# Optimization experiments

Hardware: AMD Instinct MI355X
Metric: run time of the kernel (lower is better)

## Reference

```python
import jax, jax.numpy as jnp
import numpy as np
from jax import lax

K = 3
ALPHA = 2000.0
TAU = 0.001
MAX_ITER = 100
EPS = 1e-7


def setup_inputs() -> dict:
    key = jax.random.key(0)
    x = jax.random.normal(key, (8, 2048, 32), dtype=jnp.float32)
    return {"x": x}


def _vmd(x):
    B, L, D = x.shape
    # shifted frequency grid, identical across B and D
    f = jnp.fft.fftshift(jnp.fft.fftfreq(L)).astype(x.dtype)          # [L]
    f_bld = f[None, :, None]                                           # [1,L,1]
    # nonnegative-frequency mask; torch code boolean-masks f_shifted >= 0,
    # which is uniform over B and D, so it is a weighted sum over L here
    pos = (f >= 0).astype(x.dtype)[None, None, :, None]                # [1,1,L,1]
    x_hat = jnp.fft.fftshift(jnp.fft.fft(x, axis=1), axes=1)          # [B,L,D] complex

    def step(carry, _):
        u, omega, lam = carry  # u:[B,K,L,D], omega:[B,K,D], lam:[B,L,D]
        # Gauss-Seidel mode updates (each mode sees already-updated others)
        for k_idx in range(K):
            sum_other = jnp.sum(u, axis=1) - u[:, k_idx]               # [B,L,D]
            sum_other_hat = jnp.fft.fftshift(jnp.fft.fft(sum_other, axis=1), axes=1)
            num = x_hat - sum_other_hat + lam * 0.5                    # lam added in freq domain, as in source
            den = 1.0 + 2.0 * ALPHA * (f_bld - omega[:, k_idx][:, None, :]) ** 2
            u_k = jnp.real(jnp.fft.ifft(jnp.fft.ifftshift(num / den, axes=1), axis=1))
            u = u.at[:, k_idx].set(u_k)
        # center-frequency update over nonnegative shifted frequencies
        u_hat = jnp.fft.fftshift(jnp.fft.fft(u, axis=2), axes=2)       # [B,K,L,D]
        p = (u_hat.real ** 2 + u_hat.imag ** 2) * pos                  # |u_hat|^2 masked
        omega = jnp.sum(f[None, None, :, None] * p, axis=2) / (jnp.sum(p, axis=2) + EPS)  # [B,K,D]
        # dual ascent on lambda
        lam = lam + TAU * (x - jnp.sum(u, axis=1))
        return (u, omega, lam), None

    u0 = jnp.zeros((B, K, L, D), x.dtype)
    om0 = jnp.zeros((B, K, D), x.dtype)
    lam0 = jnp.zeros((B, L, D), x.dtype)
    (u, omega, _), _ = lax.scan(jax.checkpoint(step), (u0, om0, lam0), None, length=MAX_ITER)

    # sort modes per batch element by mean center frequency
    order = jnp.argsort(jnp.mean(omega, axis=2), axis=1)               # [B,K]
    u_sorted = jnp.take_along_axis(u, order[:, :, None, None], axis=1)
    return u_sorted[:, 0], u_sorted[:, 1], u_sorted[:, 2]


def reference(x):
    return _vmd(x)
```

## Files before the change

### kernel.cpp

```cpp
#include <hip/hip_runtime.h>

#define PD(i) ((i) + ((i) >> 5))
#define BLD 524288

__device__ __forceinline__ float2 cadd(float2 a, float2 b){ return make_float2(a.x+b.x, a.y+b.y); }
__device__ __forceinline__ float2 csub(float2 a, float2 b){ return make_float2(a.x-b.x, a.y-b.y); }
__device__ __forceinline__ float2 cmul(float2 a, float2 b){ return make_float2(a.x*b.x - a.y*b.y, a.x*b.y + a.y*b.x); }
__device__ __forceinline__ float2 cmuli(float2 a, float s){ return make_float2(-s*a.y, s*a.x); }

template<int CTRL, int RM>
__device__ __forceinline__ float dpp_add(float x){
  int r = __builtin_amdgcn_update_dpp(0, __float_as_int(x), CTRL, RM, 0xf, true);
  return x + __int_as_float(r);
}
__device__ __forceinline__ float wave_sum64(float x){
  x = dpp_add<0x111,0xf>(x);
  x = dpp_add<0x112,0xf>(x);
  x = dpp_add<0x114,0xf>(x);
  x = dpp_add<0x118,0xf>(x);
  x = dpp_add<0x142,0xa>(x);
  x = dpp_add<0x143,0xc>(x);
  return x;
}

__device__ __forceinline__ float2 exbp(int addr, float2 v){
  return make_float2(
    __int_as_float(__builtin_amdgcn_ds_bpermute(addr, __float_as_int(v.x))),
    __int_as_float(__builtin_amdgcn_ds_bpermute(addr, __float_as_int(v.y))));
}
template<int PAT>
__device__ __forceinline__ float2 exswz(float2 v){
  return make_float2(
    __int_as_float(__builtin_amdgcn_ds_swizzle(__float_as_int(v.x), PAT)),
    __int_as_float(__builtin_amdgcn_ds_swizzle(__float_as_int(v.y), PAT)));
}
template<int CTRL>
__device__ __forceinline__ float2 exdpp(float2 v){
  return make_float2(
    __int_as_float(__builtin_amdgcn_update_dpp(0, __float_as_int(v.x), CTRL, 0xF, 0xF, true)),
    __int_as_float(__builtin_amdgcn_update_dpp(0, __float_as_int(v.y), CTRL, 0xF, 0xF, true)));
}

template<int SGN>
__device__ __forceinline__ void dft8(float2 a[8]) {
  const float sgn = (float)SGN;
  const float C8 = 0.70710678118654752440f;
  float2 e0=a[0], e1=a[2], e2=a[4], e3=a[6];
  float2 o0=a[1], o1=a[3], o2=a[5], o3=a[7];
  float2 t0=cadd(e0,e2), t1=csub(e0,e2), t2=cadd(e1,e3), t3=csub(e1,e3);
  float2 E0=cadd(t0,t2), E2=csub(t0,t2);
  float2 t3i=cmuli(t3,sgn);
  float2 E1=cadd(t1,t3i), E3=csub(t1,t3i);
  float2 s0=cadd(o0,o2), s1=csub(o0,o2), s2=cadd(o1,o3), s3=csub(o1,o3);
  float2 O0=cadd(s0,s2), O2=csub(s0,s2);
  float2 s3i=cmuli(s3,sgn);
  float2 O1=cadd(s1,s3i), O3=csub(s1,s3i);
  float2 w1o = make_float2(C8*(O1.x - sgn*O1.y), C8*(O1.y + sgn*O1.x));
  float2 w2o = cmuli(O2, sgn);
  float2 w3o = make_float2(-C8*(O3.x + sgn*O3.y), C8*(sgn*O3.x - O3.y));
  a[0]=cadd(E0,O0); a[4]=csub(E0,O0);
  a[1]=cadd(E1,w1o); a[5]=csub(E1,w1o);
  a[2]=cadd(E2,w2o); a[6]=csub(E2,w2o);
  a[3]=cadd(E3,w3o); a[7]=csub(E3,w3o);
}

template<int SGN>
__device__ void fft2048(float2* bufA, float2* bufB, const float2* twd, int tid)
{
  const float sgn = (float)SGN;
  {
    float2 a[8];
    #pragma unroll
    for (int j=0;j<8;j++) a[j] = bufA[PD(tid + 256*j)];
    dft8<SGN>(a);
    float2 tw = twd[tid];
    float2 w1 = make_float2(tw.x, sgn*tw.y), wj = w1;
    #pragma unroll
    for (int j=1;j<8;j++){ a[j] = cmul(a[j], wj); wj = cmul(wj, w1); }
    #pragma unroll
    for (int j=0;j<8;j++) bufB[PD(8*tid + j)] = a[j];
  }
  __syncthreads();
  {
    float2 a[8];
    #pragma unroll
    for (int j=0;j<8;j++) a[j] = bufB[PD(tid + 256*j)];
    dft8<SGN>(a);
    int p = tid >> 3, q = tid & 7;
    float2 tw = twd[p << 3];
    float2 w1 = make_float2(tw.x, sgn*tw.y), wj = w1;
    #pragma unroll
    for (int j=1;j<8;j++){ a[j] = cmul(a[j], wj); wj = cmul(wj, w1); }
    int base = q + (p << 6);
    #pragma unroll
    for (int j=0;j<8;j++) bufA[PD(base + (j<<3))] = a[j];
  }
  __syncthreads();
  {
    float2 a[8];
    #pragma unroll
    for (int j=0;j<8;j++) a[j] = bufA[PD(tid + 256*j)];
    dft8<SGN>(a);
    int p = tid >> 6, q = tid & 63;
    float2 tw = twd[p << 6];
    float2 w1 = make_float2(tw.x, sgn*tw.y), wj = w1;
    #pragma unroll
    for (int j=1;j<8;j++){ a[j] = cmul(a[j], wj); wj = cmul(wj, w1); }
    int base = q + (p << 9);
    #pragma unroll
    for (int j=0;j<8;j++) bufB[PD(base + (j<<6))] = a[j];
  }
  __syncthreads();
  {
    #pragma unroll
    for (int h=0; h<2; h++){
      int q = tid + (h<<8);
      float2 b0 = bufB[PD(q)], b1 = bufB[PD(q+512)], b2 = bufB[PD(q+1024)], b3 = bufB[PD(q+1536)];
      float2 t0=cadd(b0,b2), t1=csub(b0,b2), t2=cadd(b1,b3), t3=csub(b1,b3);
      float2 t3i=cmuli(t3,sgn);
      bufA[PD(q)]      = cadd(t0,t2);
      bufA[PD(q+512)]  = cadd(t1,t3i);
      bufA[PD(q+1024)] = csub(t0,t2);
      bufA[PD(q+1536)] = csub(t1,t3i);
    }
  }
  __syncthreads();
}

__device__ __forceinline__ void dft4p(float2 a[4]){
  float2 t0=cadd(a[0],a[2]), t1=csub(a[0],a[2]), t2=cadd(a[1],a[3]), t3=csub(a[1],a[3]);
  float2 t3i = make_float2(-t3.y, t3.x);
  a[0]=cadd(t0,t2); a[2]=csub(t0,t2);
  a[1]=cadd(t1,t3i); a[3]=csub(t1,t3i);
}

template<bool TRANSP>
__global__ __launch_bounds__(256, 1) void vmd_main(const float* __restrict__ xg,
                                                   float* __restrict__ uout,
                                                   float* __restrict__ omout)
{
  __shared__ float2 sbufA[2112];
  __shared__ float2 sbufB[2112];
  __shared__ float2 stwd[1024];
  __shared__ float  sred[24];

  float2* sS  = sbufB;
  float2* sTY = sbufA;

  const int t = threadIdx.x;
  const int lane = t & 63;
  const int w = t >> 6;
  const int blk = blockIdx.x;
  const int b = blk >> 5;
  const int d = blk & 31;
  const float inv2048 = 1.0f/2048.0f;

  for (int j = t; j < 1024; j += 256) {
    double th = 3.14159265358979323846 * (double)j / 1024.0;
    stwd[j] = make_float2((float)cos(th), (float)sin(th));
  }

  int idxs[8];
  float fl[4];
  #pragma unroll
  for (int c = 0; c < 4; c++) {
    int iL = 4*t + c;
    idxs[c]   = iL;
    idxs[c+4] = (iL == 0) ? 1024 : (2048 - iL);
    fl[c] = (float)(iL - 1024) * inv2048;
  }

  float xv[8];
  #pragma unroll
  for (int e = 0; e < 8; e++) xv[e] = xg[(b*2048 + idxs[e])*32 + d];

  #pragma unroll
  for (int e = 0; e < 8; e++) {
    float v = (idxs[e] & 1) ? -xv[e] : xv[e];
    sbufA[PD(idxs[e])] = make_float2(v, 0.0f);
  }
  __syncthreads();
  fft2048<-1>(sbufA, sbufB, stwd, t);
  float2 X[4];
  if (t == 0) X[0] = make_float2(sbufA[PD(0)].x, sbufA[PD(1024)].x);
  else        X[0] = sbufA[PD(4*t)];
  X[1] = sbufA[PD(4*t+1)];
  X[2] = sbufA[PD(4*t+2)];
  X[3] = sbufA[PD(4*t+3)];

  int r6 = ((lane&1)<<5)|((lane&2)<<3)|((lane&4)<<1)|((lane&8)>>1)|((lane&16)>>3)|((lane&32)>>5);
  const int prb = w*528 + lane;
  float2 wq[4];
  #pragma unroll
  for (int j=0;j<4;j++) wq[j] = stwd[4*lane + 256*j + w];
  float2 w2561 = stwd[8*lane];
  float2 w2562 = stwd[16*lane & 2047] ;
  float2 w2563 = cmul(w2561, w2562);
  const float sg32 = (lane&32)?-1.f:1.f, sg16 = (lane&16)?-1.f:1.f, sg8 = (lane&8)?-1.f:1.f;
  const float sg4  = (lane&4) ?-1.f:1.f, sg2  = (lane&2) ?-1.f:1.f, sg1 = (lane&1)?-1.f:1.f;
  const float2 one = make_float2(1.f, 0.f);
  float2 tw32 = (lane&32)? stwd[32*(lane&31)]  : one;
  float2 tw16 = (lane&16)? stwd[64*(lane&15)]  : one;
  float2 tw8  = (lane&8) ? stwd[128*(lane&7)]  : one;
  float2 tw4  = (lane&4) ? stwd[256*(lane&3)]  : one;
  float2 tw2  = (lane&2) ? stwd[512*(lane&1)]  : one;
  const int bp32 = ((lane^32) << 2);
  const int tyb = w*264 + r6;
  float2 tytw[4];
  #pragma unroll
  for (int r=0;r<4;r++){
    int xx2 = 2*w*(r + 4*r6);
    tytw[r] = (xx2 < 1024) ? stwd[xx2]
            : make_float2(-stwd[xx2-1024].x, -stwd[xx2-1024].y);
  }
  int slA, slB, slC, slD, slE;
  float2 phA, phB, phC, phD, phE;
  float s2A, s2B, s2C, s2D, s2E;
  {
    int ks[5];
    ks[0] = 2*t; ks[1] = 2*t+1;
    ks[2] = (t==0) ? 512 : (1024 - 2*t);
    ks[3] = 1023 - 2*t; ks[4] = 1022 - 2*t;
    int   sl[5]; float2 ph[5]; float s2[5];
    #pragma unroll
    for (int i=0;i<5;i++){
      int k1 = ks[i] >> 8, k2 = ks[i] & 255;
      sl[i] = 66*(k2 & 3) + (k2 >> 2);
      float2 P = (k1==0)? make_float2(1,0) : (k1==1)? make_float2(0,1)
               : (k1==2)? make_float2(-1,0) : make_float2(0,-1);
      ph[i] = P; s2[i] = (k1 & 1) ? -1.f : 1.f;
    }
    slA=sl[0]; slB=sl[1]; slC=sl[2]; slD=sl[3]; slE=sl[4];
    phA=ph[0]; phB=ph[1]; phC=ph[2]; phD=ph[3]; phE=ph[4];
    s2A=s2[0]; s2B=s2[1]; s2C=s2[2]; s2D=s2[3]; s2E=s2[4];
  }

  auto stageSpec = [&](float2 v0, float2 v1, float2 v2, float2 v3){
    if (t == 0) { sS[0] = make_float2(v0.x, 0.f); sS[256] = make_float2(v0.y, 0.f); }
    else        { sS[t] = v0;                     sS[512 - t] = make_float2(v0.x, -v0.y); }
    sS[528  + t] = v1;  sS[2095 - t] = make_float2(v1.x, -v1.y);
    sS[1056 + t] = v2;  sS[1567 - t] = make_float2(v2.x, -v2.y);
    sS[1584 + t] = v3;  sS[1039 - t] = make_float2(v3.x, -v3.y);
  };

  auto runFFT = [&](){
    float2 C[4];
    #pragma unroll
    for (int j=0;j<4;j++){
      float2 lo = sS[prb + 64*j];
      float2 hi = sS[prb + 64*j + 256];
      float2 Av = cadd(lo, hi), Bv = csub(lo, hi);
      float2 WB = cmul(wq[j], Bv);
      C[j] = make_float2(Av.x - WB.y, Av.y + WB.x);
    }
    dft4p(C);
    C[1] = cmul(C[1], w2561); C[2] = cmul(C[2], w2562); C[3] = cmul(C[3], w2563);
    #pragma unroll
    for (int r=0;r<4;r++){
      float2 e = exbp(bp32, C[r]);
      C[r] = cmul(make_float2(fmaf(sg32, C[r].x, e.x), fmaf(sg32, C[r].y, e.y)), tw32);
    }
    #pragma unroll
    for (int r=0;r<4;r++){
      float2 e = exswz<0x401F>(C[r]);
      C[r] = cmul(make_float2(fmaf(sg16, C[r].x, e.x), fmaf(sg16, C[r].y, e.y)), tw16);
    }
    #pragma unroll
    for (int r=0;r<4;r++){
      float2 e = exswz<0x201F>(C[r]);
      C[r] = cmul(make_float2(fmaf(sg8, C[r].x, e.x), fmaf(sg8, C[r].y, e.y)), tw8);
    }
    #pragma unroll
    for (int r=0;r<4;r++){
      float2 e = exswz<0x101F>(C[r]);
      C[r] = cmul(make_float2(fmaf(sg4, C[r].x, e.x), fmaf(sg4, C[r].y, e.y)), tw4);
    }
    #pragma unroll
    for (int r=0;r<4;r++){
      float2 e = exdpp<0x4E>(C[r]);
      C[r] = cmul(make_float2(fmaf(sg2, C[r].x, e.x), fmaf(sg2, C[r].y, e.y)), tw2);
    }
    #pragma unroll
    for (int r=0;r<4;r++){
      float2 e = exdpp<0xB1>(C[r]);
      C[r] = make_float2(fmaf(sg1, C[r].x, e.x), fmaf(sg1, C[r].y, e.y));
    }
    #pragma unroll
    for (int r=0;r<4;r++) sTY[tyb + 66*r] = cmul(C[r], tytw[r]);
  };

  auto zread = [&](int sl, float2 phi, float s2) -> float2 {
    float2 a0 = sTY[sl], a1 = sTY[sl+264], a2 = sTY[sl+528], a3 = sTY[sl+792];
    float ex = fmaf(s2, a2.x, a0.x), ey = fmaf(s2, a2.y, a0.y);
    float ox = fmaf(s2, a3.x, a1.x), oy = fmaf(s2, a3.y, a1.y);
    return make_float2(ex + phi.x*ox - phi.y*oy, ey + phi.x*oy + phi.y*ox);
  };

  float2 U[3][4], S[4];
  float lam2[8];
  #pragma unroll
  for (int c=0;c<4;c++){ S[c] = make_float2(0.f,0.f);
    #pragma unroll
    for (int k=0;k<3;k++) U[k][c] = make_float2(0.f,0.f); }
  #pragma unroll
  for (int e=0;e<8;e++) lam2[e] = 0.f;
  float om[3] = {0.f,0.f,0.f};

  for (int iter = 0; iter < 100; ++iter) {
    float sf[3], sp[3];
    #pragma unroll
    for (int k = 0; k < 3; k++) {
      float omk = om[k];
      sf[k] = 0.f; sp[k] = 0.f;
      if (t == 0) {
        float2 Uo = U[k][0];
        float n0 = X[0].x + lam2[0] - S[0].x + Uo.x;
        float n1 = X[0].y + lam2[4] - S[0].y + Uo.y;
        float d0 = -0.5f - omk, d1 = -omk;
        float u0 = n0 * __builtin_amdgcn_rcpf(fmaf(4000.f*d0, d0, 1.f));
        float u1 = n1 * __builtin_amdgcn_rcpf(fmaf(4000.f*d1, d1, 1.f));
        sp[k] += u1*u1;
        S[0].x += u0 - Uo.x; S[0].y += u1 - Uo.y;
        U[k][0] = make_float2(u0, u1);
      } else {
        float2 Uo = U[k][0];
        float bx = X[0].x - S[0].x + Uo.x;
        float by = X[0].y - S[0].y + Uo.y;
        float nl = bx + lam2[0], nh = bx + lam2[4];
        float dl = fl[0] - omk, dh = -fl[0] - omk;
        float rl = __builtin_amdgcn_rcpf(fmaf(4000.f*dl, dl, 1.f));
        float rh = __builtin_amdgcn_rcpf(fmaf(4000.f*dh, dh, 1.f));
        float ux = 0.5f*fmaf(nl, rl, nh*rh);
        float uy = 0.5f*by*(rl+rh);
        S[0].x += ux - Uo.x; S[0].y += uy - Uo.y;
        U[k][0] = make_float2(ux, uy);
        float pw = fmaf(ux, ux, uy*uy);
        sf[k] = fmaf(-fl[0], pw, sf[k]); sp[k] += pw;
      }
      #pragma unroll
      for (int c = 1; c < 4; c++) {
        float2 Uo = U[k][c];
        float bx = X[c].x - S[c].x + Uo.x;
        float by = X[c].y - S[c].y + Uo.y;
        float nl = bx + lam2[c], nh = bx + lam2[4+c];
        float dl = fl[c] - omk, dh = -fl[c] - omk;
        float rl = __builtin_amdgcn_rcpf(fmaf(4000.f*dl, dl, 1.f));
        float rh = __builtin_amdgcn_rcpf(fmaf(4000.f*dh, dh, 1.f));
        float ux = 0.5f*fmaf(nl, rl, nh*rh);
        float uy = 0.5f*by*(rl+rh);
        S[c].x += ux - Uo.x; S[c].y += uy - Uo.y;
        U[k][c] = make_float2(ux, uy);
        float pw = fmaf(ux, ux, uy*uy);
        sf[k] = fmaf(-fl[c], pw, sf[k]); sp[k] += pw;
      }
    }

    stageSpec(S[0], S[1], S[2], S[3]);

    #pragma unroll
    for (int k = 0; k < 3; k++) { sf[k] = wave_sum64(sf[k]); sp[k] = wave_sum64(sp[k]); }
    if (lane == 63) {
      #pragma unroll
      for (int k = 0; k < 3; k++) { sred[w*6 + k] = sf[k]; sred[w*6 + 3 + k] = sp[k]; }
    }
    __syncthreads();

    #pragma unroll
    for (int k = 0; k < 3; k++) {
      float a = sred[k] + sred[6+k] + sred[12+k] + sred[18+k];
      float p = sred[3+k] + sred[9+k] + sred[15+k] + sred[21+k];
      om[k] = a * __builtin_amdgcn_rcpf(p + 1e-7f);
    }

    runFFT();
    __syncthreads();

    {
      float2 zA = zread(slA, phA, s2A);
      float2 zB = zread(slB, phB, s2B);
      float2 zC = zread(slC, phC, s2C);
      float2 zD = zread(slD, phD, s2D);
      float2 zE = zread(slE, phE, s2E);
      lam2[0] = fmaf(0.0005f, xv[0] - zA.x*inv2048, lam2[0]);
      lam2[1] = fmaf(0.0005f, xv[1] + zA.y*inv2048, lam2[1]);
      lam2[2] = fmaf(0.0005f, xv[2] - zB.x*inv2048, lam2[2]);
      lam2[3] = fmaf(0.0005f, xv[3] + zB.y*inv2048, lam2[3]);
      lam2[4] = fmaf(0.0005f, xv[4] - zC.x*inv2048, lam2[4]);
      lam2[5] = fmaf(0.0005f, xv[5] + zD.y*inv2048, lam2[5]);
      lam2[6] = fmaf(0.0005f, xv[6] - zD.x*inv2048, lam2[6]);
      lam2[7] = fmaf(0.0005f, xv[7] + zE.y*inv2048, lam2[7]);
    }
  }

  #pragma unroll
  for (int k = 0; k < 3; k++) {
    stageSpec(U[k][0], U[k][1], U[k][2], U[k][3]);
    __syncthreads();
    runFFT();
    __syncthreads();
    {
      float2 zA = zread(slA, phA, s2A);
      float2 zB = zread(slB, phB, s2B);
      float2 zC = zread(slC, phC, s2C);
      float2 zD = zread(slD, phD, s2D);
      float2 zE = zread(slE, phE, s2E);
      float g[8];
      g[0] =  zA.x; g[1] = -zA.y; g[2] =  zB.x; g[3] = -zB.y;
      g[4] =  zC.x; g[5] = -zD.y; g[6] =  zD.x; g[7] = -zE.y;
      #pragma unroll
      for (int e = 0; e < 8; e++) {
        float uv = g[e] * inv2048;
        if (TRANSP) uout[(((size_t)k*8 + b)*32 + d)*2048 + idxs[e]] = uv;
        else        uout[(size_t)k*BLD + ((size_t)b*2048 + idxs[e])*32 + d] = uv;
      }
    }
  }
  if (t == 0) {
    omout[(b*3 + 0)*32 + d] = om[0];
    omout[(b*3 + 1)*32 + d] = om[1];
    omout[(b*3 + 2)*32 + d] = om[2];
  }
}

__device__ __forceinline__ void order3(const float* sm, int* sord){
  float v0=sm[0], v1=sm[1], v2=sm[2];
  int j0=0,j1=1,j2=2;
  if (v1<v0){float tv=v0;v0=v1;v1=tv;int ti=j0;j0=j1;j1=ti;}
  if (v2<v1){float tv=v1;v1=v2;v2=tv;int ti=j1;j1=j2;j2=ti;}
  if (v1<v0){float tv=v0;v0=v1;v1=tv;int ti=j0;j0=j1;j1=ti;}
  sord[0]=j0; sord[1]=j1; sord[2]=j2;
}

__global__ __launch_bounds__(256) void vmd_permute(const float* __restrict__ wsu,
                                                   const float* __restrict__ omout,
                                                   float* __restrict__ out)
{
  __shared__ float tile[32][33];
  __shared__ float sm[3];
  __shared__ int sord[3];
  int bid = blockIdx.x;
  int lt = bid & 63;
  int b = (bid >> 6) & 7;
  int kpos = bid >> 9;
  int tid = threadIdx.x;
  if (tid < 3) {
    float s = 0.f;
    for (int dd = 0; dd < 32; dd++) s += omout[(b*3 + tid)*32 + dd];
    sm[tid] = s;
  }
  __syncthreads();
  if (tid == 0) order3(sm, sord);
  __syncthreads();
  int ks = sord[kpos];
  int tr = tid >> 5, tc = tid & 31;
  for (int it = 0; it < 4; it++) {
    int dd = tr + it*8;
    tile[dd][tc] = wsu[(((size_t)ks*8 + b)*32 + dd)*2048 + lt*32 + tc];
  }
  __syncthreads();
  for (int it = 0; it < 4; it++) {
    int ll = tr + it*8;
    out[(size_t)kpos*BLD + ((size_t)b*2048 + lt*32 + ll)*32 + tc] = tile[tc][ll];
  }
}

__global__ void vmd_inplace(float* __restrict__ out, const float* __restrict__ omout)
{
  __shared__ float sm[3];
  __shared__ int sord[3];
  int r = blockIdx.x * 256 + threadIdx.x;
  int b = r >> 16;
  if (threadIdx.x < 3) {
    float s = 0.f;
    for (int dd = 0; dd < 32; dd++) s += omout[(b*3 + threadIdx.x)*32 + dd];
    sm[threadIdx.x] = s;
  }
  __syncthreads();
  if (threadIdx.x == 0) order3(sm, sord);
  __syncthreads();
  int o0 = sord[0], o1 = sord[1], o2 = sord[2];
  float v0 = out[(size_t)o0*BLD + r];
  float v1 = out[(size_t)o1*BLD + r];
  float v2 = out[(size_t)o2*BLD + r];
  out[r] = v0;
  out[(size_t)BLD + r] = v1;
  out[(size_t)2*BLD + r] = v2;
}

extern "C" void kernel_launch(void* const* d_in, const int* in_sizes, int n_in,
                              void* d_out, int out_size, void* d_ws, size_t ws_size,
                              hipStream_t stream)
{
  const float* x = (const float*)d_in[0];
  float* out = (float*)d_out;
  const size_t NU = (size_t)3 * BLD;
  size_t need = NU*4 + 768*4;
  if (ws_size >= need) {
    float* wsu  = (float*)d_ws;
    float* wsom = wsu + NU;
    vmd_main<true><<<256, 256, 0, stream>>>(x, wsu, wsom);
    vmd_permute<<<1536, 256, 0, stream>>>(wsu, wsom, out);
  } else {
    float* wsom = (float*)d_ws;
    vmd_main<false><<<256, 256, 0, stream>>>(x, out, wsom);
    vmd_inplace<<<2048, 256, 0, stream>>>(out, wsom);
  }
}
```

Before: 302.7 us.

## Drop Hermitian mirror stores and read conjugate partner directly in FFT first stage

```diff
diff --git a/kernel.cpp b/kernel.cpp
--- a/kernel.cpp
+++ b/kernel.cpp
@@ -142,10 +142,11 @@
   __shared__ float2 sbufA[2112];
   __shared__ float2 sbufB[2112];
   __shared__ float2 stwd[1024];
-  __shared__ float  sred[24];
+  __shared__ float4 sred4[6];
 
   float2* sS  = sbufB;
   float2* sTY = sbufA;
+  float*  sredf = (float*)sred4;
 
   const int t = threadIdx.x;
   const int lane = t & 63;
@@ -190,11 +191,15 @@
 
   int r6 = ((lane&1)<<5)|((lane&2)<<3)|((lane&4)<<1)|((lane&8)>>1)|((lane&16)>>3)|((lane&32)>>5);
   const int prb = w*528 + lane;
+  int hA[4];
+  #pragma unroll
+  for (int j=0;j<4;j++)
+    hA[j] = (w==0) ? (256 - 64*j - lane) : ((4-w)*528 + 255 - 64*j - lane);
   float2 wq[4];
   #pragma unroll
   for (int j=0;j<4;j++) wq[j] = stwd[4*lane + 256*j + w];
   float2 w2561 = stwd[8*lane];
-  float2 w2562 = stwd[16*lane & 2047] ;
+  float2 w2562 = stwd[16*lane & 2047];
   float2 w2563 = cmul(w2561, w2562);
   const float sg32 = (lane&32)?-1.f:1.f, sg16 = (lane&16)?-1.f:1.f, sg8 = (lane&8)?-1.f:1.f;
   const float sg4  = (lane&4) ?-1.f:1.f, sg2  = (lane&2) ?-1.f:1.f, sg1 = (lane&1)?-1.f:1.f;
@@ -237,10 +242,10 @@
 
   auto stageSpec = [&](float2 v0, float2 v1, float2 v2, float2 v3){
     if (t == 0) { sS[0] = make_float2(v0.x, 0.f); sS[256] = make_float2(v0.y, 0.f); }
-    else        { sS[t] = v0;                     sS[512 - t] = make_float2(v0.x, -v0.y); }
-    sS[528  + t] = v1;  sS[2095 - t] = make_float2(v1.x, -v1.y);
-    sS[1056 + t] = v2;  sS[1567 - t] = make_float2(v2.x, -v2.y);
-    sS[1584 + t] = v3;  sS[1039 - t] = make_float2(v3.x, -v3.y);
+    else          sS[t] = v0;
+    sS[528  + t] = v1;
+    sS[1056 + t] = v2;
+    sS[1584 + t] = v3;
   };
 
   auto runFFT = [&](){
@@ -248,8 +253,9 @@
     #pragma unroll
     for (int j=0;j<4;j++){
       float2 lo = sS[prb + 64*j];
-      float2 hi = sS[prb + 64*j + 256];
-      float2 Av = cadd(lo, hi), Bv = csub(lo, hi);
+      float2 h  = sS[hA[j]];
+      float2 Av = make_float2(lo.x + h.x, lo.y - h.y);
+      float2 Bv = make_float2(lo.x - h.x, lo.y + h.y);
       float2 WB = cmul(wq[j], Bv);
       C[j] = make_float2(Av.x - WB.y, Av.y + WB.x);
     }
@@ -267,7 +273,7 @@
     }
     #pragma unroll
     for (int r=0;r<4;r++){
-      float2 e = exswz<0x201F>(C[r]);
+      float2 e = exdpp<0x128>(C[r]);
       C[r] = cmul(make_float2(fmaf(sg8, C[r].x, e.x), fmaf(sg8, C[r].y, e.y)), tw8);
     }
     #pragma unroll
@@ -361,18 +367,20 @@
     for (int k = 0; k < 3; k++) { sf[k] = wave_sum64(sf[k]); sp[k] = wave_sum64(sp[k]); }
     if (lane == 63) {
       #pragma unroll
-      for (int k = 0; k < 3; k++) { sred[w*6 + k] = sf[k]; sred[w*6 + 3 + k] = sp[k]; }
+      for (int k = 0; k < 3; k++) { sredf[k*4 + w] = sf[k]; sredf[(3+k)*4 + w] = sp[k]; }
     }
     __syncthreads();
 
+    runFFT();
+
     #pragma unroll
     for (int k = 0; k < 3; k++) {
-      float a = sred[k] + sred[6+k] + sred[12+k] + sred[18+k];
-      float p = sred[3+k] + sred[9+k] + sred[15+k] + sred[21+k];
+      float4 A = sred4[k];
+      float4 P = sred4[3+k];
+      float a = (A.x + A.y) + (A.z + A.w);
+      float p = (P.x + P.y) + (P.z + P.w);
       om[k] = a * __builtin_amdgcn_rcpf(p + 1e-7f);
     }
-
-    runFFT();
     __syncthreads();
 
     {
```

Measured after the change: 305.7 us. Within noise of the previous version (+1.0%).
